# Kernel tuning notes

Measured on AMD Instinct MI355X. Metric: run time of the kernel, lower is better.

## Reference

```python
import jax, jax.numpy as jnp
import numpy as np
import math

B, T, N, C = 16, 24, 207, 64
E = 16   # embedding_dim
L = 3    # num_layers
NH = 4   # temporal attention heads
HD = C // NH
HOR = 12 # horizon


def _ln(x, w, b, eps=1e-5):
    m = x.mean(-1, keepdims=True)
    v = ((x - m) ** 2).mean(-1, keepdims=True)
    return (x - m) / jnp.sqrt(v + eps) * w + b


def setup_inputs():
    ks = iter(jax.random.split(jax.random.key(0), 64))
    def g(shape, s=0.1):
        return jax.random.normal(next(ks), shape, dtype=jnp.float32) * s
    inp = {}
    inp['x'] = jax.random.normal(next(ks), (B, T, N, 4), dtype=jnp.float32)
    adj = (jax.random.uniform(next(ks), (N, N)) < 0.3).astype(jnp.float32)
    inp['static_adj'] = jnp.maximum(adj, jnp.eye(N, dtype=jnp.float32))  # self-loops: no all-zero rows
    inp['node_embedding'] = g((N, E), 1.0)
    for nm in ['hour', 'day', 'weekend']:
        inp[nm + '_w'] = g((E, 1)); inp[nm + '_b'] = g((E,))
    inp['in_w'] = g((C, 1 + 4 * E)); inp['in_b'] = g((C,))
    C8 = C // 8
    inp['sa_qw'] = g((L, C8, C)); inp['sa_qb'] = g((L, C8))
    inp['sa_kw'] = g((L, C8, C)); inp['sa_kb'] = g((L, C8))
    inp['sa_vw'] = g((L, C, C)); inp['sa_vb'] = g((L, C))
    for nm in ['ta_q', 'ta_k', 'ta_v', 'ta_o']:
        inp[nm + 'w'] = g((L, C, C)); inp[nm + 'b'] = g((L, C))
    inp['ln1_w'] = jnp.ones((L, C)); inp['ln1_b'] = jnp.zeros((L, C))
    inp['ln2_w'] = jnp.ones((L, C)); inp['ln2_b'] = jnp.zeros((L, C))
    inp['ffn_w1'] = g((L, 4 * C, C)); inp['ffn_b1'] = g((L, 4 * C))
    inp['ffn_w2'] = g((L, C, 4 * C)); inp['ffn_b2'] = g((L, C))
    inp['gru_wih'] = g((2, 3 * C, C)); inp['gru_whh'] = g((2, 3 * C, C))
    inp['gru_bih'] = g((2, 3 * C)); inp['gru_bhh'] = g((2, 3 * C))
    inp['pred_w'] = g((HOR, C * T), 0.02); inp['pred_b'] = g((HOR,))
    return inp


def _forward(x, static_adj, node_embedding, hour_w, hour_b, day_w, day_b, weekend_w, weekend_b, in_w, in_b, sa_qw, sa_qb, sa_kw, sa_kb, sa_vw, sa_vb, ta_qw, ta_qb, ta_kw, ta_kb, ta_vw, ta_vb, ta_ow, ta_ob, ln1_w, ln1_b, ln2_w, ln2_b, ffn_w1, ffn_b1, ffn_w2, ffn_b2, gru_wih, gru_whh, gru_bih, gru_bhh, pred_w, pred_b):
    # eval mode: dropout = identity, no input perturbation
    flow = x[..., :1]
    hour = x[..., 1:2]; weekend = x[..., 2:3]; day = x[..., 3:4]
    node_emb = jnp.broadcast_to(node_embedding[None, None], (B, T, N, E))
    hour_emb = hour @ hour_w.T + hour_b
    day_emb = day @ day_w.T + day_b
    weekend_emb = weekend @ weekend_w.T + weekend_b
    h = jnp.concatenate([flow, node_emb, hour_emb, day_emb, weekend_emb], axis=-1)  # [B,T,N,65]
    h = h.transpose(0, 3, 2, 1)  # [B,F,N,T]
    h = jnp.einsum('of,bfnt->bont', in_w, h) + in_b[None, :, None, None]  # 1x1 conv -> [B,C,N,T]
    # positional encoding (added along channel/time, matching permute in torch)
    pos = jnp.arange(100, dtype=jnp.float32)[:, None]
    div = jnp.exp(jnp.arange(0, C, 2, dtype=jnp.float32) * (-math.log(10000.0) / C))
    pe = jnp.stack([jnp.sin(pos * div), jnp.cos(pos * div)], axis=-1).reshape(100, C)
    h = h + pe[:T].T[None, :, None, :]
    # F.normalize(adj, p=1, dim=-1) with eps clamp (torch default 1e-12)
    adj_norm = static_adj / jnp.maximum(jnp.abs(static_adj).sum(-1, keepdims=True), 1e-12)
    zero_mask = (adj_norm == 0)[None]  # [1,N,N]
    attn_mats = []
    sqrtC = math.sqrt(C); sqrtHD = math.sqrt(HD)
    for l in range(L):
        # ---- spatial attention (faithful dim-mixing reshapes of the original) ----
        hp = h.transpose(0, 1, 3, 2)  # [B,C,T,N]
        q = jnp.einsum('oc,bctn->botn', sa_qw[l], hp) + sa_qb[l][None, :, None, None]
        k = jnp.einsum('oc,bctn->botn', sa_kw[l], hp) + sa_kb[l][None, :, None, None]
        v = jnp.einsum('oc,bctn->botn', sa_vw[l], hp) + sa_vb[l][None, :, None, None]
        C8 = q.shape[1]
        q2 = q.reshape(B * T, C8, N).transpose(0, 2, 1)
        k2 = k.reshape(B * T, C8, N)
        v2 = v.reshape(B * T, C, N)
        attn = jax.nn.softmax(jnp.einsum('bnc,bcm->bnm', q2, k2) / sqrtC, axis=-1)
        attn = jnp.where(zero_mask, -jnp.inf, attn)
        attn = jax.nn.softmax(attn, axis=-1)
        sp = jnp.einsum('bcn,bmn->bcm', v2, attn).reshape(B, T, C, N).transpose(0, 2, 3, 1)  # [B,C,N,T]
        attn_mats.append(attn.reshape(B, T, N, N))
        h = h + sp
        h = _ln(h.transpose(0, 3, 2, 1), ln1_w[l], ln1_b[l]).transpose(0, 3, 2, 1)
        # ---- temporal attention (multi-head over time, per node) ----
        xt = h.transpose(0, 2, 3, 1)  # [B,N,T,C]
        def heads(w, b):
            return (xt @ w.T + b).reshape(B, N, T, NH, HD).transpose(0, 1, 3, 2, 4)
        tq = heads(ta_qw[l], ta_qb[l]); tk = heads(ta_kw[l], ta_kb[l]); tv = heads(ta_vw[l], ta_vb[l])
        scores = jnp.einsum('bnhtd,bnhsd->bnhts', tq, tk) / sqrtHD
        ta = jnp.einsum('bnhts,bnhsd->bnhtd', jax.nn.softmax(scores, axis=-1), tv)
        ta = ta.transpose(0, 1, 3, 2, 4).reshape(B, N, T, C) @ ta_ow[l].T + ta_ob[l]
        h = h + ta.transpose(0, 3, 1, 2)
        # ---- LN2 + FFN (residual taken post-LN2, as in the original) ----
        hl = _ln(h.transpose(0, 3, 2, 1), ln2_w[l], ln2_b[l])  # [B,T,N,C]
        ffn = jax.nn.relu(hl @ ffn_w1[l].T + ffn_b1[l]) @ ffn_w2[l].T + ffn_b2[l]
        h = (hl + ffn).transpose(0, 3, 2, 1)
    # ---- 2-layer GRU over time per (batch, node) ----
    seq = h.transpose(0, 2, 3, 1).reshape(B * N, T, C).transpose(1, 0, 2)  # [T,BN,C]
    for l in range(2):
        xp = jnp.einsum('tbc,gc->tbg', seq, gru_wih[l]) + gru_bih[l]
        whh = gru_whh[l]; bhh = gru_bhh[l]
        def step(hprev, xg):
            hg = hprev @ whh.T + bhh
            r = jax.nn.sigmoid(xg[:, :C] + hg[:, :C])
            z = jax.nn.sigmoid(xg[:, C:2 * C] + hg[:, C:2 * C])
            n = jnp.tanh(xg[:, 2 * C:] + r * hg[:, 2 * C:])
            hnew = (1 - z) * n + z * hprev
            return hnew, hnew
        _, seq = jax.lax.scan(step, jnp.zeros((B * N, C), dtype=seq.dtype), xp)
    h = seq.transpose(1, 0, 2).reshape(B, N, T, C).transpose(0, 3, 1, 2)  # [B,C,N,T]
    # ---- prediction head ----
    flat = h.transpose(0, 2, 1, 3).reshape(B * N, C * T)
    out = (flat @ pred_w.T + pred_b).reshape(B, N, HOR).transpose(0, 2, 1)  # [B,HOR,N]
    return out, attn_mats


def reference(x, static_adj, node_embedding, hour_w, hour_b, day_w, day_b, weekend_w, weekend_b, in_w, in_b, sa_qw, sa_qb, sa_kw, sa_kb, sa_vw, sa_vb, ta_qw, ta_qb, ta_kw, ta_kb, ta_vw, ta_vb, ta_ow, ta_ob, ln1_w, ln1_b, ln2_w, ln2_b, ffn_w1, ffn_b1, ffn_w2, ffn_b2, gru_wih, gru_whh, gru_bih, gru_bhh, pred_w, pred_b):
    out, attn_mats = _forward(x, static_adj, node_embedding, hour_w, hour_b, day_w, day_b, weekend_w, weekend_b, in_w, in_b, sa_qw, sa_qb, sa_kw, sa_kb, sa_vw, sa_vb, ta_qw, ta_qb, ta_kw, ta_kb, ta_vw, ta_vb, ta_ow, ta_ob, ln1_w, ln1_b, ln2_w, ln2_b, ffn_w1, ffn_b1, ffn_w2, ffn_b2, gru_wih, gru_whh, gru_bih, gru_bhh, pred_w, pred_b)
    return (out, jnp.stack(attn_mats))
```

## Files before the change

kernel.cpp:

```cpp
#include <hip/hip_runtime.h>
#include <math.h>

namespace {

constexpr int B = 16, T = 24, N = 207, C = 64, HOR = 12;
constexpr int BT = B * T;
constexpr int BN = B * N;
constexpr int P = B * T * N;
constexpr int NC = N * C;

constexpr size_t H_OFF = 0;
constexpr size_t A_OFF = 5087232;
constexpr size_t Q_OFF = A_OFF + 5087232;
constexpr size_t K_OFF = Q_OFF + 635904;
constexpr size_t B_OFF = K_OFF + 635904;
constexpr size_t WS_FLOATS = B_OFF + 20348928;

constexpr size_t EP_OFF = 17000000;
constexpr size_t PK_OFF = 18000000;

__device__ __forceinline__ float wsum(float v) {
#pragma unroll
  for (int off = 32; off; off >>= 1) v += __shfl_xor(v, off);
  return v;
}
__device__ __forceinline__ float wmax(float v) {
#pragma unroll
  for (int off = 32; off; off >>= 1) v = fmaxf(v, __shfl_xor(v, off));
  return v;
}
__device__ __forceinline__ float rdlane(float v, int l) {
  return __uint_as_float(__builtin_amdgcn_readlane(__float_as_uint(v), l));
}

__global__ __launch_bounds__(256) void k_embed_pack(
    const float* __restrict__ nodee, const float* __restrict__ hw,
    const float* __restrict__ hb, const float* __restrict__ dw,
    const float* __restrict__ db, const float* __restrict__ ww,
    const float* __restrict__ wb, const float* __restrict__ inw,
    const float* __restrict__ inb, float* __restrict__ ep) {
  int e = blockIdx.x * 256 + threadIdx.x;
  if (e < 13248) {
    int n = e >> 6, c = e & 63;
    const float* w = inw + c * 65 + 1;
    float a = 0.f;
#pragma unroll
    for (int i = 0; i < 16; i++) a += w[i] * nodee[n * 16 + i];
    ep[e] = a;
  } else if (e < 13568) {
    int m = e - 13248;
    int which = m >> 6, c = m & 63;
    const float* w = inw + c * 65;
    float r = 0.f;
    if (which == 0) {
      r = w[0];
    } else if (which == 1) {
#pragma unroll
      for (int i = 0; i < 16; i++) r += w[17 + i] * hw[i];
    } else if (which == 2) {
#pragma unroll
      for (int i = 0; i < 16; i++) r += w[33 + i] * dw[i];
    } else if (which == 3) {
#pragma unroll
      for (int i = 0; i < 16; i++) r += w[49 + i] * ww[i];
    } else {
      r = inb[c];
#pragma unroll
      for (int i = 0; i < 16; i++)
        r += w[17 + i] * hb[i] + w[33 + i] * db[i] + w[49 + i] * wb[i];
    }
    ep[e] = r;
  } else if (e < 15104) {
    int m = e - 13568;
    int t = m >> 6, c = m & 63;
    float dv = expf((float)(c & ~1) * (-9.210340371976184f / 64.0f));
    float ang = (float)t * dv;
    ep[e] = (c & 1) ? cosf(ang) : sinf(ang);
  }
}

__global__ __launch_bounds__(256) void k_embed(
    const float* __restrict__ x, const float* __restrict__ ep,
    float* __restrict__ H) {
  int pos = blockIdx.x * 4 + (threadIdx.x >> 6);
  int c = threadIdx.x & 63;
  int n = pos % N;
  int t = (pos / N) % T;
  const float* xv = x + (size_t)pos * 4;
  float flow = xv[0], hour = xv[1], wkend = xv[2], day = xv[3];
  float acc = ep[13504 + c] + ep[13248 + c] * flow + ep[13312 + c] * hour +
              ep[13376 + c] * day + ep[13440 + c] * wkend + ep[n * 64 + c] +
              ep[13568 + t * 64 + c];
  H[(size_t)pos * 64 + c] = acc;
}

__global__ __launch_bounds__(256) void k_pack_all(
    const float* __restrict__ w1, const float* __restrict__ w2,
    const float* __restrict__ tqw, const float* __restrict__ tkw,
    const float* __restrict__ tvw, const float* __restrict__ tow,
    float* __restrict__ pk) {
  int e = blockIdx.x * 256 + threadIdx.x;
  int l = e / 49152;
  int m = e % 49152;
  float* w1t = pk + l * 49152;
  float* w2q = w1t + 16384;
  float* taq = w2q + 16384;
  if (m < 16384) {
    int c = m >> 8, j = m & 255;
    w1t[m] = w1[l * 16384 + j * 64 + c];
  } else if (m < 32768) {
    int mm = m - 16384;
    int jq = mm >> 8, c = (mm & 255) >> 2, kk = mm & 3;
    w2q[mm] = w2[l * 16384 + c * 256 + jq * 4 + kk];
  } else {
    int m2 = m - 32768;
    int ph = m2 >> 12;
    int mm = m2 & 4095;
    int cq = mm >> 8, o = (mm & 255) >> 2, j = mm & 3;
    const float* src =
        (ph == 0 ? tqw : ph == 1 ? tkw : ph == 2 ? tvw : tow) + l * 4096;
    taq[ph * 4096 + mm] = src[o * 64 + 4 * cq + j];
  }
}

__global__ __launch_bounds__(256) void k_spatial_qkv(
    const float* __restrict__ H, const float* __restrict__ qw,
    const float* __restrict__ qb, const float* __restrict__ kw,
    const float* __restrict__ kb, const float* __restrict__ vw,
    const float* __restrict__ vb, float* __restrict__ q, float* __restrict__ k,
    float* __restrict__ v, int l) {
  __shared__ float hs[N * 65];
  int g = blockIdx.x;
  int b = g / T, t = g % T;
  const float* Hbt = H + (size_t)g * NC;
  for (int e = threadIdx.x; e < NC; e += 256) {
    int n = e >> 6, c = e & 63;
    hs[n * 65 + c] = Hbt[e];
  }
  __syncthreads();
  qw += l * 8 * 64; qb += l * 8;
  kw += l * 8 * 64; kb += l * 8;
  vw += l * 64 * 64; vb += l * 64;
  for (int e = threadIdx.x; e < 16 * N; e += 256) {
    int o = e / N, n = e % N;
    int oo = o & 7;
    const float* W = (o < 8 ? qw : kw) + oo * 64;
    float acc = (o < 8 ? qb : kb)[oo];
#pragma unroll
    for (int c = 0; c < 64; c++) acc += W[c] * hs[n * 65 + c];
    size_t oidx = ((size_t)(b * 8 + oo) * T + t) * N + n;
    if (o < 8) q[oidx] = acc; else k[oidx] = acc;
  }
  for (int e = threadIdx.x; e < 64 * N; e += 256) {
    int o = e / N, n = e % N;
    const float* W = vw + o * 64;
    float acc = vb[o];
#pragma unroll
    for (int c = 0; c < 64; c++) acc += W[c] * hs[n * 65 + c];
    v[((size_t)(b * 64 + o) * T + t) * N + n] = acc;
  }
}

__global__ __launch_bounds__(256, 2) void k_spatial_attn_pv(
    const float* __restrict__ q, const float* __restrict__ k,
    const float* __restrict__ adj, const float* __restrict__ v,
    float* __restrict__ attn_out, float* __restrict__ H) {
  __shared__ float qs[8 * 208], ks[8 * 208];
  __shared__ float vs[64 * 212];
  int g = blockIdx.x;
  const float* qg = q + (size_t)g * 1656;
  const float* kg = k + (size_t)g * 1656;
  for (int e = threadIdx.x; e < 1656; e += 256) {
    int c2 = e / N, n = e % N;
    qs[c2 * 208 + n] = qg[e];
    ks[c2 * 208 + n] = kg[e];
  }
  const float* vg = v + (size_t)g * NC;
  for (int e = threadIdx.x; e < NC; e += 256) {
    int c = e / N, n = e % N;
    vs[c * 212 + n] = vg[e];
  }
  for (int e = threadIdx.x; e < 320; e += 256) {
    int c = e / 5;
    vs[c * 212 + 207 + (e % 5)] = 0.f;
  }
  __syncthreads();
  int wave = threadIdx.x >> 6, lane = threadIdx.x & 63;
  float* Hg = H + (size_t)g * NC;
  for (int row = wave; row < N; row += 4) {
    float s[4];
    float mx = -INFINITY;
#pragma unroll
    for (int j = 0; j < 4; j++) {
      int m = lane + 64 * j;
      float acc = -INFINITY;
      if (m < N) {
        acc = 0.f;
#pragma unroll
        for (int c2 = 0; c2 < 8; c2++)
          acc += qs[c2 * 208 + row] * ks[c2 * 208 + m];
        acc *= 0.125f;
      }
      s[j] = acc;
      mx = fmaxf(mx, acc);
    }
    mx = wmax(mx);
    float sum = 0.f;
#pragma unroll
    for (int j = 0; j < 4; j++) {
      int m = lane + 64 * j;
      float e = (m < N) ? expf(s[j] - mx) : 0.f;
      s[j] = e;
      sum += e;
    }
    sum = wsum(sum);
    float inv = 1.f / sum;
    float mx2 = -INFINITY;
    bool ok[4];
#pragma unroll
    for (int j = 0; j < 4; j++) {
      int m = lane + 64 * j;
      float p = s[j] * inv;
      bool valid = (m < N) && (adj[row * N + m] != 0.0f);
      ok[j] = valid;
      s[j] = p;
      if (valid) mx2 = fmaxf(mx2, p);
    }
    mx2 = wmax(mx2);
    float sum2 = 0.f;
#pragma unroll
    for (int j = 0; j < 4; j++) {
      float e = ok[j] ? expf(s[j] - mx2) : 0.f;
      s[j] = e;
      sum2 += e;
    }
    sum2 = wsum(sum2);
    float inv2 = 1.f / sum2;
    float* orow = attn_out + ((size_t)g * N + row) * N;
#pragma unroll
    for (int j = 0; j < 4; j++) {
      int m = lane + 64 * j;
      if (m < N) orow[m] = s[j] * inv2;
    }
    const float* vrow = vs + lane * 212;
    float pacc0 = 0.f, pacc1 = 0.f, pacc2 = 0.f, pacc3 = 0.f;
#pragma unroll
    for (int j = 0; j < 3; j++) {
      float sj = s[j];
#pragma unroll
      for (int qq = 0; qq < 16; qq++) {
        int n4 = j * 16 + qq;
        float4 vv = *(const float4*)(vrow + n4 * 4);
        pacc0 += rdlane(sj, 4 * qq) * vv.x;
        pacc1 += rdlane(sj, 4 * qq + 1) * vv.y;
        pacc2 += rdlane(sj, 4 * qq + 2) * vv.z;
        pacc3 += rdlane(sj, 4 * qq + 3) * vv.w;
      }
    }
    {
      float sj = s[3];
#pragma unroll
      for (int qq = 0; qq < 4; qq++) {
        int n4 = 48 + qq;
        float4 vv = *(const float4*)(vrow + n4 * 4);
        pacc0 += rdlane(sj, 4 * qq) * vv.x;
        pacc1 += rdlane(sj, 4 * qq + 1) * vv.y;
        pacc2 += rdlane(sj, 4 * qq + 2) * vv.z;
        pacc3 += rdlane(sj, 4 * qq + 3) * vv.w;
      }
    }
    Hg[(size_t)row * 64 + lane] += inv2 * ((pacc0 + pacc1) + (pacc2 + pacc3));
  }
}

__global__ __launch_bounds__(256) void k_temporal(
    float* __restrict__ H, const float* __restrict__ taq,
    const float* __restrict__ qb, const float* __restrict__ kb,
    const float* __restrict__ vb, const float* __restrict__ ob,
    const float* __restrict__ lnw, const float* __restrict__ lnb, int l) {
  __shared__ float xs[24 * 68], qs[24 * 68], ks[24 * 68], vs[24 * 68];
  __shared__ float ss[96 * 25];
  int bn = blockIdx.x;
  int b = bn / N, n = bn % N;
  size_t base = ((size_t)b * T * N + n) * 64;
  int lane = threadIdx.x & 63, tg = threadIdx.x >> 6;
  float lw = lnw[l * 64 + lane], lb = lnb[l * 64 + lane];
  for (int t = tg; t < 24; t += 4) {
    float xv = H[base + (size_t)t * NC + lane];
    float mean = wsum(xv) * (1.f / 64.f);
    float d = xv - mean;
    float var = wsum(d * d) * (1.f / 64.f);
    xs[t * 68 + lane] = d / sqrtf(var + 1e-5f) * lw + lb;
  }
  __syncthreads();
  const float4* wq_all = (const float4*)taq;
  const float* Bm[3] = {qb + l * 64, kb + l * 64, vb + l * 64};
  float* Dm[3] = {qs, ks, vs};
#pragma unroll
  for (int ph = 0; ph < 3; ph++) {
    const float4* wq = wq_all + ph * 1024;
    float acc[6];
    float bv = Bm[ph][lane];
#pragma unroll
    for (int i = 0; i < 6; i++) acc[i] = bv;
#pragma unroll 4
    for (int cq = 0; cq < 16; cq++) {
      float4 w = wq[cq * 64 + lane];
#pragma unroll
      for (int i = 0; i < 6; i++) {
        float4 xv = *(const float4*)(&xs[(tg * 6 + i) * 68 + cq * 4]);
        acc[i] += xv.x * w.x + xv.y * w.y + xv.z * w.z + xv.w * w.w;
      }
    }
    float* dst = Dm[ph];
#pragma unroll
    for (int i = 0; i < 6; i++) dst[(tg * 6 + i) * 68 + lane] = acc[i];
  }
  __syncthreads();
  for (int e = threadIdx.x; e < 2304; e += 256) {
    int u = e % 24, t = (e / 24) % 24, h = e / 576;
    float a = 0.f;
#pragma unroll
    for (int dq = 0; dq < 4; dq++) {
      float4 qv = *(const float4*)(&qs[t * 68 + h * 16 + dq * 4]);
      float4 kv = *(const float4*)(&ks[u * 68 + h * 16 + dq * 4]);
      a += qv.x * kv.x + qv.y * kv.y + qv.z * kv.z + qv.w * kv.w;
    }
    ss[(h * 24 + t) * 25 + u] = a * 0.25f;
  }
  __syncthreads();
  if (threadIdx.x < 96) {
    float* row = ss + threadIdx.x * 25;
    float mx = -INFINITY;
#pragma unroll
    for (int u = 0; u < 24; u++) mx = fmaxf(mx, row[u]);
    float sum = 0.f;
#pragma unroll
    for (int u = 0; u < 24; u++) {
      float e2 = expf(row[u] - mx);
      row[u] = e2;
      sum += e2;
    }
    float inv = 1.f / sum;
#pragma unroll
    for (int u = 0; u < 24; u++) row[u] *= inv;
  }
  __syncthreads();
  {
    int h = lane >> 4;
    float acc2[6];
#pragma unroll
    for (int i = 0; i < 6; i++) acc2[i] = 0.f;
    for (int u = 0; u < 24; u++) {
      float vsv = vs[u * 68 + lane];
#pragma unroll
      for (int i = 0; i < 6; i++)
        acc2[i] += ss[(h * 24 + (tg * 6 + i)) * 25 + u] * vsv;
    }
#pragma unroll
    for (int i = 0; i < 6; i++) qs[(tg * 6 + i) * 68 + lane] = acc2[i];
  }
  __syncthreads();
  {
    const float4* wo = wq_all + 3 * 1024;
    float acc[6];
    float bv = ob[l * 64 + lane];
#pragma unroll
    for (int i = 0; i < 6; i++) acc[i] = bv;
#pragma unroll 4
    for (int cq = 0; cq < 16; cq++) {
      float4 w = wo[cq * 64 + lane];
#pragma unroll
      for (int i = 0; i < 6; i++) {
        float4 xv = *(const float4*)(&qs[(tg * 6 + i) * 68 + cq * 4]);
        acc[i] += xv.x * w.x + xv.y * w.y + xv.z * w.z + xv.w * w.w;
      }
    }
#pragma unroll
    for (int i = 0; i < 6; i++)
      H[base + (size_t)(tg * 6 + i) * NC + lane] =
          xs[(tg * 6 + i) * 68 + lane] + acc[i];
  }
}

__global__ __launch_bounds__(256) void k_ffn(
    float* __restrict__ H, const float* __restrict__ lnw,
    const float* __restrict__ lnb, const float* __restrict__ w1t,
    const float* __restrict__ b1, const float* __restrict__ w2q,
    const float* __restrict__ b2, int l) {
  __shared__ float xs[24 * 66];
  __shared__ float hids[24 * 260];
  int bn = blockIdx.x;
  int b = bn / N, n = bn % N;
  size_t base = ((size_t)b * T * N + n) * 64;
  int lane = threadIdx.x & 63, tg = threadIdx.x >> 6;
  for (int t = tg; t < 24; t += 4) {
    float xv = H[base + (size_t)t * NC + lane];
    float mean = wsum(xv) * (1.f / 64.f);
    float d = xv - mean;
    float var = wsum(d * d) * (1.f / 64.f);
    xs[t * 66 + lane] = d / sqrtf(var + 1e-5f) * lnw[l * 64 + lane] + lnb[l * 64 + lane];
  }
  __syncthreads();
  int j0 = lane * 4;
  float4 b4 = *(const float4*)(b1 + l * 256 + j0);
  float a0[6], a1[6], a2[6], a3[6];
#pragma unroll
  for (int i = 0; i < 6; i++) { a0[i] = b4.x; a1[i] = b4.y; a2[i] = b4.z; a3[i] = b4.w; }
  for (int c = 0; c < 64; c++) {
    float4 w4 = *(const float4*)(w1t + c * 256 + j0);
#pragma unroll
    for (int i = 0; i < 6; i++) {
      float xv = xs[(tg * 6 + i) * 66 + c];
      a0[i] += xv * w4.x;
      a1[i] += xv * w4.y;
      a2[i] += xv * w4.z;
      a3[i] += xv * w4.w;
    }
  }
#pragma unroll
  for (int i = 0; i < 6; i++) {
    int t = tg * 6 + i;
    float4 r = make_float4(fmaxf(a0[i], 0.f), fmaxf(a1[i], 0.f),
                           fmaxf(a2[i], 0.f), fmaxf(a3[i], 0.f));
    *(float4*)(&hids[t * 260 + j0]) = r;
  }
  __syncthreads();
  const float4* w2q4 = (const float4*)w2q;
  float acc[6];
#pragma unroll
  for (int i = 0; i < 6; i++) acc[i] = 0.f;
  for (int jq = 0; jq < 64; jq++) {
    float4 w = w2q4[jq * 64 + lane];
#pragma unroll
    for (int i = 0; i < 6; i++) {
      float4 hv = *(const float4*)(&hids[(tg * 6 + i) * 260 + jq * 4]);
      acc[i] += hv.x * w.x + hv.y * w.y + hv.z * w.z + hv.w * w.w;
    }
  }
  float bias = b2[l * 64 + lane];
#pragma unroll
  for (int i = 0; i < 6; i++) {
    int t = tg * 6 + i;
    H[base + (size_t)t * NC + lane] = xs[t * 66 + lane] + bias + acc[i];
  }
}

__global__ __launch_bounds__(256) void k_gru_xp(
    const float* __restrict__ X, const float* __restrict__ wih,
    const float* __restrict__ bih, float* __restrict__ xp, int l) {
  __shared__ float ws_[192 * 65];
  __shared__ float xv[16 * 64];
  int p0 = blockIdx.x * 16;
  for (int e = threadIdx.x; e < 192 * 64; e += 256) {
    int gI = e >> 6, c = e & 63;
    ws_[gI * 65 + c] = wih[l * 12288 + e];
  }
  for (int e = threadIdx.x; e < 16 * 64; e += 256) {
    int s = e >> 6, c = e & 63;
    int p = p0 + s;
    int t = p / BN, bn = p % BN;
    float val;
    if (l == 0) {
      int b = bn / N, n = bn % N;
      val = X[(((size_t)b * T + t) * N + n) * 64 + c];
    } else {
      val = X[(size_t)p * 64 + c];
    }
    xv[e] = val;
  }
  __syncthreads();
  for (int e = threadIdx.x; e < 16 * 192; e += 256) {
    int s = e / 192, gI = e % 192;
    float acc = bih[l * 192 + gI];
#pragma unroll
    for (int c = 0; c < 64; c++) acc += xv[s * 64 + c] * ws_[gI * 65 + c];
    xp[((size_t)(p0 + s)) * 192 + gI] = acc;
  }
}

__global__ __launch_bounds__(256) void k_gru_scan(
    const float* __restrict__ xp, const float* __restrict__ whh,
    const float* __restrict__ bhh, float* __restrict__ seq_out, int l) {
  constexpr int S = 8;
  __shared__ float hprev[S][64];
  __shared__ float hg[3][S][64];
  __shared__ float xpbuf[2][S * 192];
  int bn0 = blockIdx.x * S;
  int lane = threadIdx.x & 63;
  int wv = threadIdx.x >> 6;

  float4 w4[16];
  if (wv < 3) {
    const float* wr = whh + l * 12288 + (wv * 64 + lane) * 64;
#pragma unroll
    for (int j = 0; j < 16; j++) w4[j] = *(const float4*)(wr + j * 4);
  }
  float b_r = bhh[l * 192 + lane];
  float b_z = bhh[l * 192 + 64 + lane];
  float b_n = bhh[l * 192 + 128 + lane];

  for (int e = threadIdx.x; e < S * 64; e += 256) ((float*)hprev)[e] = 0.f;
  {
    const float* src = xp + (size_t)bn0 * 192;
    for (int e = threadIdx.x; e < S * 192; e += 256) xpbuf[0][e] = src[e];
  }
  __syncthreads();

  for (int t = 0; t < T; t++) {
    int cur = t & 1;
    if (wv < 3) {
      float acc[S];
#pragma unroll
      for (int s = 0; s < S; s++) acc[s] = 0.f;
#pragma unroll
      for (int j = 0; j < 16; j++) {
        float4 w = w4[j];
#pragma unroll
        for (int s = 0; s < S; s++) {
          float4 hb = *(const float4*)(&hprev[s][j * 4]);
          acc[s] += w.x * hb.x + w.y * hb.y + w.z * hb.z + w.w * hb.w;
        }
      }
#pragma unroll
      for (int s = 0; s < S; s++) hg[wv][s][lane] = acc[s];
    } else {
      if (t + 1 < T) {
        const float* src = xp + ((size_t)(t + 1) * BN + bn0) * 192;
        float* dst = xpbuf[(t + 1) & 1];
        for (int e = lane * 4; e < S * 192; e += 256) {
          *(float4*)(dst + e) = *(const float4*)(src + e);
        }
      }
    }
    __syncthreads();
#pragma unroll
    for (int ii = 0; ii < 2; ii++) {
      int s = wv + 4 * ii;
      const float* xr = &xpbuf[cur][s * 192];
      float r = 1.f / (1.f + expf(-(xr[lane] + hg[0][s][lane] + b_r)));
      float z = 1.f / (1.f + expf(-(xr[64 + lane] + hg[1][s][lane] + b_z)));
      float nn = tanhf(xr[128 + lane] + r * (hg[2][s][lane] + b_n));
      float hp = hprev[s][lane];
      float hnew = (1.f - z) * nn + z * hp;
      hprev[s][lane] = hnew;
      seq_out[((size_t)t * BN + bn0 + s) * 64 + lane] = hnew;
    }
    __syncthreads();
  }
}

__global__ __launch_bounds__(256) void k_pred(
    const float* __restrict__ seq2, const float* __restrict__ pw,
    const float* __restrict__ pb, float* __restrict__ out) {
  __shared__ float s_[1536];
  int bn = blockIdx.x;
  int b = bn / N, n = bn % N;
  for (int e = threadIdx.x; e < 1536; e += 256) {
    int t = e >> 6, c = e & 63;
    s_[c * 24 + t] = seq2[((size_t)t * BN + bn) * 64 + c];
  }
  __syncthreads();
  int wave = threadIdx.x >> 6, lane = threadIdx.x & 63;
  for (int hor = wave; hor < 12; hor += 4) {
    const float* w = pw + hor * 1536;
    float acc = 0.f;
#pragma unroll 4
    for (int kk = lane; kk < 1536; kk += 64) acc += s_[kk] * w[kk];
    acc = wsum(acc);
    if (lane == 0) out[(size_t)b * (HOR * N) + hor * N + n] = acc + pb[hor];
  }
}

}

extern "C" void kernel_launch(void* const* d_in, const int* in_sizes, int n_in,
                              void* d_out, int out_size, void* d_ws, size_t ws_size,
                              hipStream_t stream) {
  const float* x       = (const float*)d_in[0];
  const float* adj     = (const float*)d_in[1];
  const float* nodee   = (const float*)d_in[2];
  const float* hour_w  = (const float*)d_in[3];
  const float* hour_b  = (const float*)d_in[4];
  const float* day_w   = (const float*)d_in[5];
  const float* day_b   = (const float*)d_in[6];
  const float* wk_w    = (const float*)d_in[7];
  const float* wk_b    = (const float*)d_in[8];
  const float* in_w    = (const float*)d_in[9];
  const float* in_b    = (const float*)d_in[10];
  const float* sa_qw   = (const float*)d_in[11];
  const float* sa_qb   = (const float*)d_in[12];
  const float* sa_kw   = (const float*)d_in[13];
  const float* sa_kb   = (const float*)d_in[14];
  const float* sa_vw   = (const float*)d_in[15];
  const float* sa_vb   = (const float*)d_in[16];
  const float* ta_qw   = (const float*)d_in[17];
  const float* ta_qb   = (const float*)d_in[18];
  const float* ta_kw   = (const float*)d_in[19];
  const float* ta_kb   = (const float*)d_in[20];
  const float* ta_vw   = (const float*)d_in[21];
  const float* ta_vb   = (const float*)d_in[22];
  const float* ta_ow   = (const float*)d_in[23];
  const float* ta_ob   = (const float*)d_in[24];
  const float* ln1_w   = (const float*)d_in[25];
  const float* ln1_b   = (const float*)d_in[26];
  const float* ln2_w   = (const float*)d_in[27];
  const float* ln2_b   = (const float*)d_in[28];
  const float* ffn_w1  = (const float*)d_in[29];
  const float* ffn_b1  = (const float*)d_in[30];
  const float* ffn_w2  = (const float*)d_in[31];
  const float* ffn_b2  = (const float*)d_in[32];
  const float* gru_wih = (const float*)d_in[33];
  const float* gru_whh = (const float*)d_in[34];
  const float* gru_bih = (const float*)d_in[35];
  const float* gru_bhh = (const float*)d_in[36];
  const float* pred_w  = (const float*)d_in[37];
  const float* pred_b  = (const float*)d_in[38];

  if (ws_size < WS_FLOATS * sizeof(float)) return;

  float* ws   = (float*)d_ws;
  float* H    = ws + H_OFF;
  float* bufA = ws + A_OFF;
  float* q    = ws + Q_OFF;
  float* k    = ws + K_OFF;
  float* bufB = ws + B_OFF;

  float* out       = (float*)d_out;
  float* attn_base = out + (size_t)B * HOR * N;

  float* v   = bufB;
  float* xp  = bufB;
  float* ep  = bufB + EP_OFF;
  float* pk  = bufB + PK_OFF;

  k_embed_pack<<<60, 256, 0, stream>>>(nodee, hour_w, hour_b, day_w, day_b,
                                       wk_w, wk_b, in_w, in_b, ep);
  k_embed<<<P / 4, 256, 0, stream>>>(x, ep, H);
  k_pack_all<<<576, 256, 0, stream>>>(ffn_w1, ffn_w2, ta_qw, ta_kw, ta_vw,
                                      ta_ow, pk);

  for (int l = 0; l < 3; l++) {
    float* attn_l = attn_base + (size_t)l * BT * N * N;
    float* w1t = pk + (size_t)l * 49152;
    float* w2q = w1t + 16384;
    float* taq = w2q + 16384;
    k_spatial_qkv<<<BT, 256, 0, stream>>>(H, sa_qw, sa_qb, sa_kw, sa_kb, sa_vw,
                                          sa_vb, q, k, v, l);
    k_spatial_attn_pv<<<BT, 256, 0, stream>>>(q, k, adj, v, attn_l, H);
    k_temporal<<<BN, 256, 0, stream>>>(H, taq, ta_qb, ta_kb, ta_vb, ta_ob,
                                       ln1_w, ln1_b, l);
    k_ffn<<<BN, 256, 0, stream>>>(H, ln2_w, ln2_b, w1t, ffn_b1, w2q, ffn_b2, l);
  }

  k_gru_xp<<<P / 16, 256, 0, stream>>>(H, gru_wih, gru_bih, xp, 0);
  k_gru_scan<<<BN / 8, 256, 0, stream>>>(xp, gru_whh, gru_bhh, bufA, 0);
  k_gru_xp<<<P / 16, 256, 0, stream>>>(bufA, gru_wih, gru_bih, xp, 1);
  k_gru_scan<<<BN / 8, 256, 0, stream>>>(xp, gru_whh, gru_bhh, H, 1);

  k_pred<<<BN, 256, 0, stream>>>(H, pred_w, pred_b, out);
}
```

Before: 2.165 ms.

## Block spatial attention PV over four rows per wave and split rows across blocks

The spatial attention kernel now launches a second grid dimension so each (b,t) group's 207 rows are split across two blocks. Within a block, each wave computes softmax for four rows at a time and stages the final probabilities in shared memory. It then does the P·V product with one float4 load of V reused across all four rows, replacing the per-row readlane broadcasts. The aim is more parallelism and fewer LDS loads and readlane instructions per output, at the cost of loading Q, K and V into shared memory twice per group and more LDS per block.

```diff
diff --git a/kernel.cpp b/kernel.cpp
--- a/kernel.cpp
+++ b/kernel.cpp
@@ -28,9 +28,6 @@
 #pragma unroll
   for (int off = 32; off; off >>= 1) v = fmaxf(v, __shfl_xor(v, off));
   return v;
-}
-__device__ __forceinline__ float rdlane(float v, int l) {
-  return __uint_as_float(__builtin_amdgcn_readlane(__float_as_uint(v), l));
 }
 
 __global__ __launch_bounds__(256) void k_embed_pack(
@@ -167,7 +164,10 @@
     float* __restrict__ attn_out, float* __restrict__ H) {
   __shared__ float qs[8 * 208], ks[8 * 208];
   __shared__ float vs[64 * 212];
+  __shared__ float pbuf[4][4][212];
   int g = blockIdx.x;
+  int rbeg = blockIdx.y * 104;
+  int rend = min(rbeg + 104, N);
   const float* qg = q + (size_t)g * 1656;
   const float* kg = k + (size_t)g * 1656;
   for (int e = threadIdx.x; e < 1656; e += 256) {
@@ -187,89 +187,85 @@
   __syncthreads();
   int wave = threadIdx.x >> 6, lane = threadIdx.x & 63;
   float* Hg = H + (size_t)g * NC;
-  for (int row = wave; row < N; row += 4) {
-    float s[4];
-    float mx = -INFINITY;
-#pragma unroll
-    for (int j = 0; j < 4; j++) {
-      int m = lane + 64 * j;
-      float acc = -INFINITY;
-      if (m < N) {
-        acc = 0.f;
-#pragma unroll
-        for (int c2 = 0; c2 < 8; c2++)
-          acc += qs[c2 * 208 + row] * ks[c2 * 208 + m];
-        acc *= 0.125f;
+  const float* vrow = vs + lane * 212;
+  for (int round = 0; round < 7; round++) {
+    int row0 = rbeg + round * 16 + wave * 4;
+#pragma unroll
+    for (int i = 0; i < 4; i++) {
+      int row = row0 + i;
+      if (row < rend) {
+        float s[4];
+        float mx = -INFINITY;
+#pragma unroll
+        for (int j = 0; j < 4; j++) {
+          int m = lane + 64 * j;
+          float acc = -INFINITY;
+          if (m < N) {
+            acc = 0.f;
+#pragma unroll
+            for (int c2 = 0; c2 < 8; c2++)
+              acc += qs[c2 * 208 + row] * ks[c2 * 208 + m];
+            acc *= 0.125f;
+          }
+          s[j] = acc;
+          mx = fmaxf(mx, acc);
+        }
+        mx = wmax(mx);
+        float sum = 0.f;
+#pragma unroll
+        for (int j = 0; j < 4; j++) {
+          int m = lane + 64 * j;
+          float e = (m < N) ? expf(s[j] - mx) : 0.f;
+          s[j] = e;
+          sum += e;
+        }
+        sum = wsum(sum);
+        float inv = 1.f / sum;
+        float mx2 = -INFINITY;
+        bool ok[4];
+#pragma unroll
+        for (int j = 0; j < 4; j++) {
+          int m = lane + 64 * j;
+          float p = s[j] * inv;
+          bool valid = (m < N) && (adj[row * N + m] != 0.0f);
+          ok[j] = valid;
+          s[j] = p;
+          if (valid) mx2 = fmaxf(mx2, p);
+        }
+        mx2 = wmax(mx2);
+        float sum2 = 0.f;
+#pragma unroll
+        for (int j = 0; j < 4; j++) {
+          float e = ok[j] ? expf(s[j] - mx2) : 0.f;
+          s[j] = e;
+          sum2 += e;
+        }
+        sum2 = wsum(sum2);
+        float inv2 = 1.f / sum2;
+        float* orow = attn_out + ((size_t)g * N + row) * N;
+#pragma unroll
+        for (int j = 0; j < 4; j++) {
+          int m = lane + 64 * j;
+          float pfin = s[j] * inv2;
+          if (m < N) orow[m] = pfin;
+          if (m < 212) pbuf[wave][i][m] = pfin;
+        }
       }
-      s[j] = acc;
-      mx = fmaxf(mx, acc);
-    }
-    mx = wmax(mx);
-    float sum = 0.f;
-#pragma unroll
-    for (int j = 0; j < 4; j++) {
-      int m = lane + 64 * j;
-      float e = (m < N) ? expf(s[j] - mx) : 0.f;
-      s[j] = e;
-      sum += e;
-    }
-    sum = wsum(sum);
-    float inv = 1.f / sum;
-    float mx2 = -INFINITY;
-    bool ok[4];
-#pragma unroll
-    for (int j = 0; j < 4; j++) {
-      int m = lane + 64 * j;
-      float p = s[j] * inv;
-      bool valid = (m < N) && (adj[row * N + m] != 0.0f);
-      ok[j] = valid;
-      s[j] = p;
-      if (valid) mx2 = fmaxf(mx2, p);
-    }
-    mx2 = wmax(mx2);
-    float sum2 = 0.f;
-#pragma unroll
-    for (int j = 0; j < 4; j++) {
-      float e = ok[j] ? expf(s[j] - mx2) : 0.f;
-      s[j] = e;
-      sum2 += e;
-    }
-    sum2 = wsum(sum2);
-    float inv2 = 1.f / sum2;
-    float* orow = attn_out + ((size_t)g * N + row) * N;
-#pragma unroll
-    for (int j = 0; j < 4; j++) {
-      int m = lane + 64 * j;
-      if (m < N) orow[m] = s[j] * inv2;
-    }
-    const float* vrow = vs + lane * 212;
-    float pacc0 = 0.f, pacc1 = 0.f, pacc2 = 0.f, pacc3 = 0.f;
-#pragma unroll
-    for (int j = 0; j < 3; j++) {
-      float sj = s[j];
-#pragma unroll
-      for (int qq = 0; qq < 16; qq++) {
-        int n4 = j * 16 + qq;
-        float4 vv = *(const float4*)(vrow + n4 * 4);
-        pacc0 += rdlane(sj, 4 * qq) * vv.x;
-        pacc1 += rdlane(sj, 4 * qq + 1) * vv.y;
-        pacc2 += rdlane(sj, 4 * qq + 2) * vv.z;
-        pacc3 += rdlane(sj, 4 * qq + 3) * vv.w;
+    }
+    float acc[4] = {0.f, 0.f, 0.f, 0.f};
+    for (int n4 = 0; n4 < 52; n4++) {
+      float4 vv = *(const float4*)(vrow + n4 * 4);
+#pragma unroll
+      for (int i = 0; i < 4; i++) {
+        float4 pv = *(const float4*)(&pbuf[wave][i][n4 * 4]);
+        acc[i] += pv.x * vv.x + pv.y * vv.y + pv.z * vv.z + pv.w * vv.w;
       }
     }
-    {
-      float sj = s[3];
-#pragma unroll
-      for (int qq = 0; qq < 4; qq++) {
-        int n4 = 48 + qq;
-        float4 vv = *(const float4*)(vrow + n4 * 4);
-        pacc0 += rdlane(sj, 4 * qq) * vv.x;
-        pacc1 += rdlane(sj, 4 * qq + 1) * vv.y;
-        pacc2 += rdlane(sj, 4 * qq + 2) * vv.z;
-        pacc3 += rdlane(sj, 4 * qq + 3) * vv.w;
-      }
-    }
-    Hg[(size_t)row * 64 + lane] += inv2 * ((pacc0 + pacc1) + (pacc2 + pacc3));
+#pragma unroll
+    for (int i = 0; i < 4; i++) {
+      int row = row0 + i;
+      if (row < rend) Hg[(size_t)row * 64 + lane] += acc[i];
+    }
   }
 }
 
@@ -647,7 +643,7 @@
     float* taq = w2q + 16384;
     k_spatial_qkv<<<BT, 256, 0, stream>>>(H, sa_qw, sa_qb, sa_kw, sa_kb, sa_vw,
                                           sa_vb, q, k, v, l);
-    k_spatial_attn_pv<<<BT, 256, 0, stream>>>(q, k, adj, v, attn_l, H);
+    k_spatial_attn_pv<<<dim3(BT, 2), 256, 0, stream>>>(q, k, adj, v, attn_l, H);
     k_temporal<<<BN, 256, 0, stream>>>(H, taq, ta_qb, ta_kb, ta_vb, ta_ob,
                                        ln1_w, ln1_b, l);
     k_ffn<<<BN, 256, 0, stream>>>(H, ln2_w, ln2_b, w1t, ffn_b1, w2q, ffn_b2, l);
```

New measurement: 1.993 ms. 7.9% less time.
